# Performance work log

Measured on AMD Instinct MI355X. Metric: run time of the kernel, lower is better.

## Reference

```python
import jax, jax.numpy as jnp
import numpy as np

WS = 32          # window_size
STRIDE = 16
OUTPUT = 224
GRADE_N = 6

def _dct_mat(size):
    i = np.arange(size)[:, None]
    j = np.arange(size)[None, :]
    scale = np.where(i == 0, np.sqrt(1.0 / size), np.sqrt(2.0 / size))
    return (scale * np.cos((j + 0.5) * np.pi * i / size)).astype(np.float32)

def _gen_filter(start, end, size):
    i = np.arange(size)[:, None]
    j = np.arange(size)[None, :]
    s = i + j
    return np.where((s > end) | (s < start), 0.0, 1.0).astype(np.float32)

# constant (non-learnable) buffers, derived from init hyperparams
_D = jnp.asarray(_dct_mat(WS))                       # [32,32]
_LEVEL_FILT = jnp.asarray(_gen_filter(0, WS * 2, WS))  # level_fliter=[0] -> band (0, 64)
_grade_filts = np.stack([_gen_filter(WS * 2.0 / GRADE_N * i, WS * 2.0 / GRADE_N * (i + 1), WS)
                         for i in range(GRADE_N)])    # [G,32,32]
_ft_num = _grade_filts.sum(axis=(1, 2))               # per-filter normalizer
_weights = (2.0 ** np.arange(GRADE_N)).astype(np.float32)  # w=1, *=2 each pass
_GRADE_FILT_SCALED = jnp.asarray(_grade_filts * (_weights / _ft_num)[:, None, None])  # [G,32,32]

def _unfold(x):
    # x: [B,C,H,W] -> patches [B,L,C,ws,ws], L row-major over (oh, ow), matching torch Unfold
    B, C, H, W = x.shape
    nH = (H - WS) // STRIDE + 1
    nW = (W - WS) // STRIDE + 1
    r = jnp.arange(nH) * STRIDE
    c = jnp.arange(nW) * STRIDE
    rows = r[:, None, None, None] + jnp.arange(WS)[None, None, :, None]  # [nH,1,ws,1]
    cols = c[None, :, None, None] + jnp.arange(WS)[None, None, None, :]  # [1,nW,1,ws]
    p = x[:, :, rows, cols]                       # [B,C,nH,nW,ws,ws]
    p = jnp.transpose(p, (0, 2, 3, 1, 4, 5))      # [B,nH,nW,C,ws,ws]
    return p.reshape(B, nH * nW, C, WS, WS)

def setup_inputs() -> dict:
    key = jax.random.key(0)
    x = jax.random.normal(key, (16, 3, 512, 512), dtype=jnp.float32)
    return {"x": x}

def reference(x):
    B, C, H, W = x.shape
    patches = _unfold(x)                          # [B,L,C,32,32]
    x_dct = _D @ patches @ _D.T                   # batched 32x32 DCT

    # level branch (level_N=1): filter is all-pass band (0,64) but applied faithfully
    level_y = _D.T @ (x_dct * _LEVEL_FILT) @ _D   # [B,L,C,32,32]

    # grading: sum_g w_g/ft_g * sum_{c,i,j} filt_g * log(|dct|+1)
    lx = jnp.log(jnp.abs(x_dct) + 1.0)
    grade = jnp.einsum('blcij,gij->bl', lx, _GRADE_FILT_SCALED)  # [B,L]

    idx = jnp.argsort(grade, axis=-1)             # ascending
    b = jnp.arange(B)
    minmin_i  = idx[:, 0]
    minmin_i1 = idx[:, 1]    # B > 1 branch
    maxmax_i  = idx[:, -1]
    maxmax_i1 = idx[:, -2]   # B > 1 branch

    # gather single patch per image; fold0 with one block == reshape to [B,C,32,32]
    x_minmin  = level_y[b, minmin_i]
    x_maxmax  = level_y[b, maxmax_i]
    x_minmin1 = level_y[b, minmin_i1]
    x_maxmax1 = level_y[b, maxmax_i1]
    return (x_minmin, x_maxmax, x_minmin1, x_maxmax1)
```

## Files before the change

kernel.cpp:

```cpp
#include <hip/hip_runtime.h>
#include <cstdint>

typedef _Float16 f16x8 __attribute__((ext_vector_type(8)));
typedef float    f32x4 __attribute__((ext_vector_type(4)));

constexpr double kPI  = 3.14159265358979323846264338327950288;
constexpr double kLN2 = 0.69314718055994530941723212145818;
constexpr double cos_poly(double x) {
    double x2 = x * x, term = 1.0, sum = 1.0;
    for (int n = 1; n <= 13; ++n) { term *= -x2 / double((2 * n - 1) * (2 * n)); sum += term; }
    return sum;
}
constexpr double cos_idx(int a) {
    a &= 127;
    if (a <= 32)  return  cos_poly(a * kPI / 64.0);
    if (a <= 64)  return -cos_poly((64 - a) * kPI / 64.0);
    if (a <= 96)  return -cos_poly((a - 64) * kPI / 64.0);
    return cos_poly((128 - a) * kPI / 64.0);
}
constexpr double csqrt(double v) {
    double x = 1.0;
    for (int i = 0; i < 60; ++i) x = 0.5 * (x + v / x);
    return x;
}
constexpr unsigned short d2h(double dv) {
    float f = (float)dv;
    double v = (double)f;
    unsigned short s = 0;
    if (v < 0.0) { s = 0x8000; v = -v; }
    if (v == 0.0) return s;
    int e = 0;
    while (v >= 2.0) { v *= 0.5; ++e; }
    while (v < 1.0)  { v *= 2.0; --e; }
    double m = (v - 1.0) * 1024.0;
    int mi = (int)m;
    double fr = m - (double)mi;
    if (fr > 0.5 || (fr == 0.5 && (mi & 1))) ++mi;
    int ef = e + 15;
    if (mi == 1024) { mi = 0; ++ef; }
    return (unsigned short)(s | (ef << 10) | mi);
}
struct __align__(16) HTab { unsigned short h[1024]; };
constexpr HTab make_H() {
    HTab t{};
    const double s0 = csqrt(1.0 / 32.0);
    for (int tl = 0; tl < 2; ++tl)
        for (int lane = 0; lane < 64; ++lane) {
            const int m  = 16 * tl + (lane & 15);
            const int k0 = (lane >> 4) * 8;
            const double sc = (m == 0) ? s0 : 0.25;
            for (int j = 0; j < 8; ++j)
                t.h[(tl * 64 + lane) * 8 + j] = d2h(sc * cos_idx(((2 * (k0 + j) + 1) * m) & 127));
        }
    return t;
}
struct FTab { float f[64]; };
constexpr FTab make_F() {
    FTab t{};
    const int lo[6] = {0, 11, 22, 32, 43, 54};
    const int hi[6] = {10, 21, 32, 42, 53, 62};
    const int n [6] = {66, 187, 306, 286, 165, 45};
    for (int s = 0; s < 64; ++s) {
        double acc = 0.0, w = 1.0;
        for (int g = 0; g < 6; ++g) { if (s >= lo[g] && s <= hi[g]) acc += w / double(n[g]); w *= 2.0; }
        t.f[s] = (float)(acc * kLN2);
    }
    return t;
}
__device__ constexpr HTab cH = make_H();
__device__ constexpr FTab cF = make_F();

#define NP  15376
#define NPC 46128
#define LPB 961
#define TP  36
#define CPX 2883


__global__ __launch_bounds__(128, 4) void k_grade(const float* __restrict__ x,
                                                  float* __restrict__ out) {
    __shared__ __align__(16) float sT[2][32 * TP];
    __shared__ float sF[64];
    const int tid  = threadIdx.x;
    const int wv   = tid >> 6, lane = tid & 63;
    const int quad = lane >> 4, n = lane & 15;
    if (tid < 64) sF[tid] = cF.f[tid];

    const int bid = blockIdx.x;
    const int vb  = (bid & 7) * CPX + (bid >> 3);
    const int tc   = vb * 2 + wv;
    const int task = tc / 3, c = tc - task * 3;
    const int b  = task / LPB, l = task - b * LPB;
    const int ph = l / 31, pw = l - ph * 31;

    const f16x8* DF = (const f16x8*)cH.h;
    const f16x8 d0 = DF[lane], d1 = DF[64 + lane];

    const float* pp = x + (size_t)(b * 3 + c) * 262144
                        + (size_t)(ph * 16 + n) * 512 + pw * 16 + quad * 8;
    const float4 v0 = *(const float4*)(pp);
    const float4 v1 = *(const float4*)(pp + 4);
    const float4 v2 = *(const float4*)(pp + 16 * 512);
    const float4 v3 = *(const float4*)(pp + 16 * 512 + 4);
    f16x8 p0, p1;
    p0[0]=(_Float16)v0.x; p0[1]=(_Float16)v0.y; p0[2]=(_Float16)v0.z; p0[3]=(_Float16)v0.w;
    p0[4]=(_Float16)v1.x; p0[5]=(_Float16)v1.y; p0[6]=(_Float16)v1.z; p0[7]=(_Float16)v1.w;
    p1[0]=(_Float16)v2.x; p1[1]=(_Float16)v2.y; p1[2]=(_Float16)v2.z; p1[3]=(_Float16)v2.w;
    p1[4]=(_Float16)v3.x; p1[5]=(_Float16)v3.y; p1[6]=(_Float16)v3.z; p1[7]=(_Float16)v3.w;

    const f32x4 z4 = {0.f, 0.f, 0.f, 0.f};
    f32x4 t00 = __builtin_amdgcn_mfma_f32_16x16x32_f16(d0, p0, z4, 0, 0, 0);
    f32x4 t01 = __builtin_amdgcn_mfma_f32_16x16x32_f16(d0, p1, z4, 0, 0, 0);
    f32x4 t10 = __builtin_amdgcn_mfma_f32_16x16x32_f16(d1, p0, z4, 0, 0, 0);
    f32x4 t11 = __builtin_amdgcn_mfma_f32_16x16x32_f16(d1, p1, z4, 0, 0, 0);

    float* S = sT[wv];
    #pragma unroll
    for (int r = 0; r < 4; ++r) {
        S[(quad * 4 + r) * TP + n]           = t00[r];
        S[(quad * 4 + r) * TP + 16 + n]      = t01[r];
        S[(16 + quad * 4 + r) * TP + n]      = t10[r];
        S[(16 + quad * 4 + r) * TP + 16 + n] = t11[r];
    }
    __syncthreads();

    f16x8 a0, a1;
    {
        const float* rp = &S[n * TP + quad * 8];
        const float4 x0 = *(const float4*)(rp);
        const float4 x1 = *(const float4*)(rp + 4);
        const float4 x2 = *(const float4*)(rp + 16 * TP);
        const float4 x3 = *(const float4*)(rp + 16 * TP + 4);
        a0[0]=(_Float16)x0.x; a0[1]=(_Float16)x0.y; a0[2]=(_Float16)x0.z; a0[3]=(_Float16)x0.w;
        a0[4]=(_Float16)x1.x; a0[5]=(_Float16)x1.y; a0[6]=(_Float16)x1.z; a0[7]=(_Float16)x1.w;
        a1[0]=(_Float16)x2.x; a1[1]=(_Float16)x2.y; a1[2]=(_Float16)x2.z; a1[3]=(_Float16)x2.w;
        a1[4]=(_Float16)x3.x; a1[5]=(_Float16)x3.y; a1[6]=(_Float16)x3.z; a1[7]=(_Float16)x3.w;
    }

    f32x4 q00 = __builtin_amdgcn_mfma_f32_16x16x32_f16(a0, d0, z4, 0, 0, 0);
    f32x4 q01 = __builtin_amdgcn_mfma_f32_16x16x32_f16(a0, d1, z4, 0, 0, 0);
    f32x4 q10 = __builtin_amdgcn_mfma_f32_16x16x32_f16(a1, d0, z4, 0, 0, 0);
    f32x4 q11 = __builtin_amdgcn_mfma_f32_16x16x32_f16(a1, d1, z4, 0, 0, 0);

    const int sb = quad * 4 + n;
    float W[12];
    #pragma unroll
    for (int t2 = 0; t2 < 3; ++t2)
        #pragma unroll
        for (int r = 0; r < 4; ++r) W[t2 * 4 + r] = sF[sb + 16 * t2 + r];

    float gsum = 0.f;
    #pragma unroll
    for (int r = 0; r < 4; ++r) {
        gsum = fmaf(__log2f(fabsf(q00[r]) + 1.f), W[r],     gsum);
        gsum = fmaf(__log2f(fabsf(q01[r]) + 1.f), W[4 + r], gsum);
        gsum = fmaf(__log2f(fabsf(q10[r]) + 1.f), W[4 + r], gsum);
        gsum = fmaf(__log2f(fabsf(q11[r]) + 1.f), W[8 + r], gsum);
    }
    #pragma unroll
    for (int off = 32; off > 0; off >>= 1) gsum += __shfl_down(gsum, off, 64);
    if (lane == 0) out[b * 3072 + l * 3 + c] = gsum;
}

__global__ __launch_bounds__(256) void k_selgather(const float* __restrict__ x,
                                                   float* out) {
    __shared__ unsigned long long smx1[256], smx2[256], smn1[256], smn2[256];
    __shared__ int ssel[4];
    const int b = blockIdx.x, tid = threadIdx.x;
    unsigned long long mx1 = 0, mx2 = 0, mn1 = ~0ULL, mn2 = ~0ULL;
    for (int l = tid; l < LPB; l += 256) {
        const float* pp = out + b * 3072 + l * 3;
        float gr = pp[0] + pp[1] + pp[2];
        unsigned int bits = __float_as_uint(gr);
        unsigned long long k = ((unsigned long long)bits << 32) | (unsigned int)l;
        if (k > mx1) { mx2 = mx1; mx1 = k; } else if (k > mx2) { mx2 = k; }
        if (k < mn1) { mn2 = mn1; mn1 = k; } else if (k < mn2) { mn2 = k; }
    }
    smx1[tid] = mx1; smx2[tid] = mx2; smn1[tid] = mn1; smn2[tid] = mn2;
    for (int off = 128; off > 0; off >>= 1) {
        __syncthreads();
        if (tid < off) {
            unsigned long long a1 = smx1[tid], a2 = smx2[tid], b1 = smx1[tid + off], b2 = smx2[tid + off];
            unsigned long long lo = a1 < b1 ? a1 : b1, hi = a1 < b1 ? b1 : a1;
            unsigned long long c2 = a2 > b2 ? a2 : b2;
            smx1[tid] = hi; smx2[tid] = lo > c2 ? lo : c2;
            a1 = smn1[tid]; a2 = smn2[tid]; b1 = smn1[tid + off]; b2 = smn2[tid + off];
            lo = a1 < b1 ? a1 : b1; hi = a1 < b1 ? b1 : a1;
            c2 = a2 < b2 ? a2 : b2;
            smn1[tid] = lo; smn2[tid] = hi < c2 ? hi : c2;
        }
    }
    __syncthreads();
    if (tid == 0) {
        ssel[0] = (int)(smn1[0] & 0xffffffffu);
        ssel[1] = (int)(smx1[0] & 0xffffffffu);
        ssel[2] = (int)(smn2[0] & 0xffffffffu);
        ssel[3] = (int)(smx2[0] & 0xffffffffu);
    }
    __syncthreads();

    #pragma unroll
    for (int it = 0; it < 12; ++it) {
        const int q  = it * 256 + tid;
        const int o  = q / 768;
        const int r2 = q - o * 768;
        const int c  = r2 >> 8;
        const int p  = r2 & 255;
        const int i  = p >> 3, j4 = p & 7;
        const int l  = ssel[o];
        const int lh = l / 31;
        const int r0 = lh * 16, c0 = (l - lh * 31) * 16;
        const float4 v = *(const float4*)(x + ((size_t)(b * 3 + c) * 512 + r0 + i) * 512 + c0 + 4 * j4);
        *(float4*)(out + (size_t)o * 49152 + b * 3072 + c * 1024 + i * 32 + 4 * j4) = v;
    }
}

extern "C" void kernel_launch(void* const* d_in, const int* in_sizes, int n_in,
                              void* d_out, int out_size, void* d_ws, size_t ws_size,
                              hipStream_t stream) {
    const float* x = (const float*)d_in[0];
    float* out     = (float*)d_out;
    (void)d_ws; (void)ws_size;
    k_grade    <<<NPC / 2, 128, 0, stream>>>(x, out);
    k_selgather<<<16,      256, 0, stream>>>(x, out);
}
```

Measured before the change: 104.3 us.

## Process all three channels of a patch in one single-wave block

Result: faster. 102.2 us (-2.0%).

```diff
diff --git a/kernel.cpp b/kernel.cpp
--- a/kernel.cpp
+++ b/kernel.cpp
@@ -71,62 +71,72 @@
 __device__ constexpr FTab cF = make_F();
 
 #define NP  15376
-#define NPC 46128
 #define LPB 961
 #define TP  36
-#define CPX 2883
-
-
-__global__ __launch_bounds__(128, 4) void k_grade(const float* __restrict__ x,
-                                                  float* __restrict__ out) {
-    __shared__ __align__(16) float sT[2][32 * TP];
+#define CPX 1922
+
+
+__global__ __launch_bounds__(64, 2) void k_grade(const float* __restrict__ x,
+                                                 float* __restrict__ out) {
+    __shared__ __align__(16) float sT[3][32 * TP];
     __shared__ float sF[64];
-    const int tid  = threadIdx.x;
-    const int wv   = tid >> 6, lane = tid & 63;
+    const int lane = threadIdx.x;
     const int quad = lane >> 4, n = lane & 15;
-    if (tid < 64) sF[tid] = cF.f[tid];
-
-    const int bid = blockIdx.x;
-    const int vb  = (bid & 7) * CPX + (bid >> 3);
-    const int tc   = vb * 2 + wv;
-    const int task = tc / 3, c = tc - task * 3;
+    sF[lane] = cF.f[lane];
+
+    const int bid  = blockIdx.x;
+    const int task = (bid & 7) * CPX + (bid >> 3);
     const int b  = task / LPB, l = task - b * LPB;
     const int ph = l / 31, pw = l - ph * 31;
 
     const f16x8* DF = (const f16x8*)cH.h;
     const f16x8 d0 = DF[lane], d1 = DF[64 + lane];
 
-    const float* pp = x + (size_t)(b * 3 + c) * 262144
-                        + (size_t)(ph * 16 + n) * 512 + pw * 16 + quad * 8;
-    const float4 v0 = *(const float4*)(pp);
-    const float4 v1 = *(const float4*)(pp + 4);
-    const float4 v2 = *(const float4*)(pp + 16 * 512);
-    const float4 v3 = *(const float4*)(pp + 16 * 512 + 4);
-    f16x8 p0, p1;
-    p0[0]=(_Float16)v0.x; p0[1]=(_Float16)v0.y; p0[2]=(_Float16)v0.z; p0[3]=(_Float16)v0.w;
-    p0[4]=(_Float16)v1.x; p0[5]=(_Float16)v1.y; p0[6]=(_Float16)v1.z; p0[7]=(_Float16)v1.w;
-    p1[0]=(_Float16)v2.x; p1[1]=(_Float16)v2.y; p1[2]=(_Float16)v2.z; p1[3]=(_Float16)v2.w;
-    p1[4]=(_Float16)v3.x; p1[5]=(_Float16)v3.y; p1[6]=(_Float16)v3.z; p1[7]=(_Float16)v3.w;
+    const float* pbase = x + (size_t)b * 786432
+                           + (size_t)(ph * 16 + n) * 512 + pw * 16 + quad * 8;
+    f16x8 p0[3], p1[3];
+    #pragma unroll
+    for (int c = 0; c < 3; ++c) {
+        const float* pp = pbase + c * 262144;
+        const float4 v0 = *(const float4*)(pp);
+        const float4 v1 = *(const float4*)(pp + 4);
+        const float4 v2 = *(const float4*)(pp + 16 * 512);
+        const float4 v3 = *(const float4*)(pp + 16 * 512 + 4);
+        p0[c][0]=(_Float16)v0.x; p0[c][1]=(_Float16)v0.y; p0[c][2]=(_Float16)v0.z; p0[c][3]=(_Float16)v0.w;
+        p0[c][4]=(_Float16)v1.x; p0[c][5]=(_Float16)v1.y; p0[c][6]=(_Float16)v1.z; p0[c][7]=(_Float16)v1.w;
+        p1[c][0]=(_Float16)v2.x; p1[c][1]=(_Float16)v2.y; p1[c][2]=(_Float16)v2.z; p1[c][3]=(_Float16)v2.w;
+        p1[c][4]=(_Float16)v3.x; p1[c][5]=(_Float16)v3.y; p1[c][6]=(_Float16)v3.z; p1[c][7]=(_Float16)v3.w;
+    }
 
     const f32x4 z4 = {0.f, 0.f, 0.f, 0.f};
-    f32x4 t00 = __builtin_amdgcn_mfma_f32_16x16x32_f16(d0, p0, z4, 0, 0, 0);
-    f32x4 t01 = __builtin_amdgcn_mfma_f32_16x16x32_f16(d0, p1, z4, 0, 0, 0);
-    f32x4 t10 = __builtin_amdgcn_mfma_f32_16x16x32_f16(d1, p0, z4, 0, 0, 0);
-    f32x4 t11 = __builtin_amdgcn_mfma_f32_16x16x32_f16(d1, p1, z4, 0, 0, 0);
-
-    float* S = sT[wv];
-    #pragma unroll
-    for (int r = 0; r < 4; ++r) {
-        S[(quad * 4 + r) * TP + n]           = t00[r];
-        S[(quad * 4 + r) * TP + 16 + n]      = t01[r];
-        S[(16 + quad * 4 + r) * TP + n]      = t10[r];
-        S[(16 + quad * 4 + r) * TP + 16 + n] = t11[r];
-    }
-    __syncthreads();
-
-    f16x8 a0, a1;
-    {
-        const float* rp = &S[n * TP + quad * 8];
+    #pragma unroll
+    for (int c = 0; c < 3; ++c) {
+        f32x4 t00 = __builtin_amdgcn_mfma_f32_16x16x32_f16(d0, p0[c], z4, 0, 0, 0);
+        f32x4 t01 = __builtin_amdgcn_mfma_f32_16x16x32_f16(d0, p1[c], z4, 0, 0, 0);
+        f32x4 t10 = __builtin_amdgcn_mfma_f32_16x16x32_f16(d1, p0[c], z4, 0, 0, 0);
+        f32x4 t11 = __builtin_amdgcn_mfma_f32_16x16x32_f16(d1, p1[c], z4, 0, 0, 0);
+        float* S = sT[c];
+        #pragma unroll
+        for (int r = 0; r < 4; ++r) {
+            S[(quad * 4 + r) * TP + n]           = t00[r];
+            S[(quad * 4 + r) * TP + 16 + n]      = t01[r];
+            S[(16 + quad * 4 + r) * TP + n]      = t10[r];
+            S[(16 + quad * 4 + r) * TP + 16 + n] = t11[r];
+        }
+    }
+
+    const int sb = quad * 4 + n;
+    float W[12];
+    #pragma unroll
+    for (int t2 = 0; t2 < 3; ++t2)
+        #pragma unroll
+        for (int r = 0; r < 4; ++r) W[t2 * 4 + r] = sF[sb + 16 * t2 + r];
+
+    float gsum = 0.f;
+    #pragma unroll
+    for (int c = 0; c < 3; ++c) {
+        f16x8 a0, a1;
+        const float* rp = &sT[c][n * TP + quad * 8];
         const float4 x0 = *(const float4*)(rp);
         const float4 x1 = *(const float4*)(rp + 4);
         const float4 x2 = *(const float4*)(rp + 16 * TP);
@@ -135,31 +145,23 @@
         a0[4]=(_Float16)x1.x; a0[5]=(_Float16)x1.y; a0[6]=(_Float16)x1.z; a0[7]=(_Float16)x1.w;
         a1[0]=(_Float16)x2.x; a1[1]=(_Float16)x2.y; a1[2]=(_Float16)x2.z; a1[3]=(_Float16)x2.w;
         a1[4]=(_Float16)x3.x; a1[5]=(_Float16)x3.y; a1[6]=(_Float16)x3.z; a1[7]=(_Float16)x3.w;
-    }
-
-    f32x4 q00 = __builtin_amdgcn_mfma_f32_16x16x32_f16(a0, d0, z4, 0, 0, 0);
-    f32x4 q01 = __builtin_amdgcn_mfma_f32_16x16x32_f16(a0, d1, z4, 0, 0, 0);
-    f32x4 q10 = __builtin_amdgcn_mfma_f32_16x16x32_f16(a1, d0, z4, 0, 0, 0);
-    f32x4 q11 = __builtin_amdgcn_mfma_f32_16x16x32_f16(a1, d1, z4, 0, 0, 0);
-
-    const int sb = quad * 4 + n;
-    float W[12];
-    #pragma unroll
-    for (int t2 = 0; t2 < 3; ++t2)
+
+        f32x4 q00 = __builtin_amdgcn_mfma_f32_16x16x32_f16(a0, d0, z4, 0, 0, 0);
+        f32x4 q01 = __builtin_amdgcn_mfma_f32_16x16x32_f16(a0, d1, z4, 0, 0, 0);
+        f32x4 q10 = __builtin_amdgcn_mfma_f32_16x16x32_f16(a1, d0, z4, 0, 0, 0);
+        f32x4 q11 = __builtin_amdgcn_mfma_f32_16x16x32_f16(a1, d1, z4, 0, 0, 0);
+
         #pragma unroll
-        for (int r = 0; r < 4; ++r) W[t2 * 4 + r] = sF[sb + 16 * t2 + r];
-
-    float gsum = 0.f;
-    #pragma unroll
-    for (int r = 0; r < 4; ++r) {
-        gsum = fmaf(__log2f(fabsf(q00[r]) + 1.f), W[r],     gsum);
-        gsum = fmaf(__log2f(fabsf(q01[r]) + 1.f), W[4 + r], gsum);
-        gsum = fmaf(__log2f(fabsf(q10[r]) + 1.f), W[4 + r], gsum);
-        gsum = fmaf(__log2f(fabsf(q11[r]) + 1.f), W[8 + r], gsum);
+        for (int r = 0; r < 4; ++r) {
+            gsum = fmaf(__log2f(fabsf(q00[r]) + 1.f), W[r],     gsum);
+            gsum = fmaf(__log2f(fabsf(q01[r]) + 1.f), W[4 + r], gsum);
+            gsum = fmaf(__log2f(fabsf(q10[r]) + 1.f), W[4 + r], gsum);
+            gsum = fmaf(__log2f(fabsf(q11[r]) + 1.f), W[8 + r], gsum);
+        }
     }
     #pragma unroll
     for (int off = 32; off > 0; off >>= 1) gsum += __shfl_down(gsum, off, 64);
-    if (lane == 0) out[b * 3072 + l * 3 + c] = gsum;
+    if (lane == 0) out[b * 3072 + l] = gsum;
 }
 
 __global__ __launch_bounds__(256) void k_selgather(const float* __restrict__ x,
@@ -169,8 +171,7 @@
     const int b = blockIdx.x, tid = threadIdx.x;
     unsigned long long mx1 = 0, mx2 = 0, mn1 = ~0ULL, mn2 = ~0ULL;
     for (int l = tid; l < LPB; l += 256) {
-        const float* pp = out + b * 3072 + l * 3;
-        float gr = pp[0] + pp[1] + pp[2];
+        float gr = out[b * 3072 + l];
         unsigned int bits = __float_as_uint(gr);
         unsigned long long k = ((unsigned long long)bits << 32) | (unsigned int)l;
         if (k > mx1) { mx2 = mx1; mx1 = k; } else if (k > mx2) { mx2 = k; }
@@ -221,6 +222,6 @@
     const float* x = (const float*)d_in[0];
     float* out     = (float*)d_out;
     (void)d_ws; (void)ws_size;
-    k_grade    <<<NPC / 2, 128, 0, stream>>>(x, out);
-    k_selgather<<<16,      256, 0, stream>>>(x, out);
-}
+    k_grade    <<<NP, 64, 0, stream>>>(x, out);
+    k_selgather<<<16, 256, 0, stream>>>(x, out);
+}
```
